# Kernel optimization log

Hardware: AMD Instinct MI355X
Metric: run time of the kernel (lower is better)

## Reference

```python
import jax, jax.numpy as jnp
import numpy as np

N_NODES = 50000
N_EDGES = 600000
N_REL = 64
D = 128
N_LAYERS = 2


def setup_inputs() -> dict:
    key = jax.random.key(0)
    k1, k2, k3, k4, k5, k6 = jax.random.split(key, 6)
    return {
        "entity_table": jax.random.normal(k1, (N_NODES, D), jnp.float32) * 0.05,
        "relation_table": jax.random.normal(k2, (N_REL, D), jnp.float32) * 0.05,
        "W": jax.random.normal(k3, (N_LAYERS, 2 * D, D), jnp.float32) * 0.05,
        "b": jnp.zeros((N_LAYERS, D), jnp.float32),
        "edge_dst": jax.random.randint(k4, (N_EDGES,), 0, N_NODES),
        "edge_nbr": jax.random.randint(k5, (N_EDGES,), 0, N_NODES),
        "edge_rel": jax.random.randint(k6, (N_EDGES,), 0, N_REL),
    }


def _segment_softmax(score, seg, num_segments):
    # numerically stable per-destination-node softmax over incoming edges
    smax = jax.ops.segment_max(score, seg, num_segments=num_segments)
    ex = jnp.exp(score - smax[seg])
    denom = jax.ops.segment_sum(ex, seg, num_segments=num_segments)
    return ex / denom[seg]


def reference(entity_table, relation_table, W, b, edge_dst, edge_nbr, edge_rel):
    n_nodes, d = entity_table.shape
    n_layers = W.shape[0]
    deg = jax.ops.segment_sum(jnp.ones_like(edge_dst, dtype=entity_table.dtype),
                              edge_dst, num_segments=n_nodes)
    has_nbr = (deg > 0)[:, None]  # [N,1]

    # relation-attentive query uses the BASE entity embedding of the dst node
    # (the torch code passes entity_embedder(current_node) each layer)
    q = jnp.tanh(entity_table[edge_dst] + relation_table[edge_rel])  # [E,d]

    prev = entity_table
    for l in range(n_layers):
        nbr_emb = prev[edge_nbr]                      # [E,d] gather
        score = jnp.sum(nbr_emb * q, axis=-1)         # [E]
        alpha = _segment_softmax(score, edge_dst, n_nodes)
        neigh = jax.ops.segment_sum(alpha[:, None] * nbr_emb, edge_dst,
                                    num_segments=n_nodes)  # [N,d]
        h = jnp.concatenate([prev, neigh], axis=-1) @ W[l] + b[l]
        h = jax.nn.leaky_relu(h)                      # LeakyReLU slope 0.01
        h = h / jnp.linalg.norm(h, axis=-1, keepdims=True)
        # nodes with no neighbours keep their base entity embedding
        prev = jnp.where(has_nbr, h, entity_table)
    return prev
```

## Files before the change

### kernel.cpp

```cpp
#include <hip/hip_runtime.h>
#include <math.h>

#define NN 50000
#define NE 600000
#define NR 64
#define DD 128
#define FB 586

typedef __attribute__((ext_vector_type(2))) _Float16 h2;
typedef __attribute__((ext_vector_type(4))) _Float16 h4;
typedef __attribute__((ext_vector_type(8))) _Float16 h8;
typedef __attribute__((ext_vector_type(4))) float f32x4;


__device__ __forceinline__ h2 tanh_h2(h2 x) {
    const h2 C5 = {(_Float16)0.1333333333f,  (_Float16)0.1333333333f};
    const h2 C3 = {(_Float16)-0.3333333333f, (_Float16)-0.3333333333f};
    const h2 ONE = {(_Float16)1.f, (_Float16)1.f};
    h2 x2 = x * x;
    h2 p = x2 * C5 + C3;
    p = x2 * p + ONE;
    return x * p;
}

template <int CTRL, int ROW_MASK>
__device__ __forceinline__ float dpp_add(float x) {
    int xi = __builtin_bit_cast(int, x);
    int yi = __builtin_amdgcn_update_dpp(0, xi, CTRL, ROW_MASK, 0xF, true);
    return x + __builtin_bit_cast(float, yi);
}


__global__ __launch_bounds__(256) void prep_k(const float* __restrict__ ent,
                                              const float* __restrict__ rel,
                                              const float* __restrict__ W,
                                              const int* __restrict__ edst,
                                              const int* __restrict__ enbr,
                                              const int* __restrict__ erel,
                                              _Float16* __restrict__ Ah,
                                              _Float16* __restrict__ relh,
                                              _Float16* __restrict__ wp,
                                              int* __restrict__ deg,
                                              int* __restrict__ bucket) {
    int b = blockIdx.x;
    if (b < FB) {
        int e = (b * 256 + threadIdx.x) * 4;
        if (e < NE) {
            int4 d  = *(const int4*)&edst[e];
            int4 nb = *(const int4*)&enbr[e];
            int4 rl = *(const int4*)&erel[e];
            int r0 = atomicAdd(&deg[d.x], 1);
            int r1 = atomicAdd(&deg[d.y], 1);
            int r2 = atomicAdd(&deg[d.z], 1);
            int r3 = atomicAdd(&deg[d.w], 1);
            if (r0 < 64) bucket[d.x * 64 + r0] = nb.x | (rl.x << 16);
            if (r1 < 64) bucket[d.y * 64 + r1] = nb.y | (rl.y << 16);
            if (r2 < 64) bucket[d.z * 64 + r2] = nb.z | (rl.z << 16);
            if (r3 < 64) bucket[d.w * 64 + r3] = nb.w | (rl.w << 16);
        }
    } else if (b < FB + 6250) {
        int tid = (b - FB) * 256 + threadIdx.x;
        int node = tid >> 5, c = tid & 31;
        float4 v = *(const float4*)&ent[(size_t)node * DD + c * 4];
        h4 o = {(_Float16)v.x, (_Float16)v.y, (_Float16)v.z, (_Float16)v.w};
        *(h4*)&Ah[(size_t)node * 256 + c * 4] = o;
    } else if (b < FB + 6258) {
        int tid = (b - FB - 6250) * 256 + threadIdx.x;
        float4 v = *(const float4*)&rel[tid * 4];
        h4 o = {(_Float16)v.x, (_Float16)v.y, (_Float16)v.z, (_Float16)v.w};
        *(h4*)&relh[tid * 4] = o;
    } else {
        int tid = (b - FB - 6258) * 256 + threadIdx.x;
        int lane = tid & 63;
        int ct   = (tid >> 6) & 7;
        int ks   = (tid >> 9) & 7;
        int l    = tid >> 12;
        int q = lane >> 4, n = lane & 15;
        const float* Wl = W + (size_t)l * 256 * 128;
        _Float16* dst = wp + ((((size_t)l * 8 + ks) * 8 + ct) * 64 + lane) * 8;
#pragma unroll
        for (int j = 0; j < 8; ++j) {
            int k = ks * 32 + q * 8 + j;
            dst[j] = (_Float16)Wl[(size_t)k * 128 + ct * 16 + n];
        }
    }
}


__global__ __launch_bounds__(256) void agg_k(const _Float16* __restrict__ Ah,
                                             const _Float16* __restrict__ Aq,
                                             const _Float16* __restrict__ relh,
                                             const int* __restrict__ deg_,
                                             const int* __restrict__ bucket,
                                             _Float16* __restrict__ Ah_out) {
    int lane = threadIdx.x & 63;
    int grp  = lane >> 4;
    int t16  = lane & 15;
    int wid  = threadIdx.x >> 6;
    int node = blockIdx.x * 4 + wid;
    int dg = deg_[node];

    unsigned dof = (unsigned)t16 * 8u;
    h8 qv = *(const h8*)&Aq[(unsigned)node * 256u + dof];
    h2 q0 = {qv[0], qv[1]}, q1 = {qv[2], qv[3]}, q2 = {qv[4], qv[5]}, q3 = {qv[6], qv[7]};

    float l = 0.f;
    h2 acc0 = {(_Float16)0.f, (_Float16)0.f};
    h2 acc1 = acc0, acc2 = acc0, acc3 = acc0;

    if (dg > 0) {
        int e0 = node * 64;
        int e1 = e0 + dg;
        int iters = (dg + 3) >> 2;
        int last = e1 - 1;
        int ei = e0 + grp;

        int pk_c = bucket[min(ei, last)];
        h8 nb_c = *(const h8*)&Ah[(unsigned)(pk_c & 0xFFFF) * 256u + dof];
        h8 rl_c = *(const h8*)&relh[(unsigned)(pk_c >> 16) * 128u + dof];
        int pk_n = bucket[min(ei + 4, last)];

#pragma unroll 2
        for (int it = 0; it < iters; ++it) {
            int pk_n2 = bucket[min(ei + 8, last)];
            h8 nb_n = *(const h8*)&Ah[(unsigned)(pk_n & 0xFFFF) * 256u + dof];
            h8 rl_n = *(const h8*)&relh[(unsigned)(pk_n >> 16) * 128u + dof];

            h2 n0 = {nb_c[0], nb_c[1]}, n1 = {nb_c[2], nb_c[3]};
            h2 n2 = {nb_c[4], nb_c[5]}, n3 = {nb_c[6], nb_c[7]};
            h2 r0 = {rl_c[0], rl_c[1]}, r1 = {rl_c[2], rl_c[3]};
            h2 r2 = {rl_c[4], rl_c[5]}, r3 = {rl_c[6], rl_c[7]};

            h2 sd = n0 * tanh_h2(q0 + r0);
            sd = n1 * tanh_h2(q1 + r1) + sd;
            sd = n2 * tanh_h2(q2 + r2) + sd;
            sd = n3 * tanh_h2(q3 + r3) + sd;
            float s = (float)sd.x + (float)sd.y;

            s = dpp_add<0x111, 0xF>(s);
            s = dpp_add<0x112, 0xF>(s);
            s = dpp_add<0x114, 0xF>(s);
            s = dpp_add<0x118, 0xF>(s);
            int si = __builtin_amdgcn_ds_swizzle(__builtin_bit_cast(int, s), 0x1F0);
            s = __builtin_bit_cast(float, si);

            float p = (ei < e1) ? __expf(s) : 0.f;
            l += p;
            _Float16 ph = (_Float16)p;
            h2 p2 = {ph, ph};
            acc0 = p2 * n0 + acc0;
            acc1 = p2 * n1 + acc1;
            acc2 = p2 * n2 + acc2;
            acc3 = p2 * n3 + acc3;

            ei += 4;
            pk_c = pk_n; pk_n = pk_n2;
            nb_c = nb_n; rl_c = rl_n;
        }

#pragma unroll
        for (int off = 16; off <= 32; off <<= 1) {
            acc0 += __builtin_bit_cast(h2, __shfl_xor(__builtin_bit_cast(int, acc0), off, 64));
            acc1 += __builtin_bit_cast(h2, __shfl_xor(__builtin_bit_cast(int, acc1), off, 64));
            acc2 += __builtin_bit_cast(h2, __shfl_xor(__builtin_bit_cast(int, acc2), off, 64));
            acc3 += __builtin_bit_cast(h2, __shfl_xor(__builtin_bit_cast(int, acc3), off, 64));
            l += __shfl_xor(l, off, 64);
        }
    }

    float inv = (dg > 0) ? __builtin_amdgcn_rcpf(l) : 0.f;
    if (grp == 0) {
        _Float16 ih = (_Float16)inv;
        h2 iv = {ih, ih};
        h2 o0 = acc0 * iv, o1 = acc1 * iv, o2 = acc2 * iv, o3 = acc3 * iv;
        h8 o = {o0.x, o0.y, o1.x, o1.y, o2.x, o2.y, o3.x, o3.y};
        *(h8*)&Ah_out[(unsigned)node * 256u + 128u + dof] = o;
    }
}


template <bool LAST>
__global__ __launch_bounds__(256) void upd_k(const _Float16* __restrict__ Ah,
                                             const _Float16* __restrict__ wp,
                                             const float* __restrict__ bl,
                                             const int* __restrict__ deg_,
                                             const float* __restrict__ ent,
                                             float* __restrict__ out,
                                             _Float16* __restrict__ Ahn) {
    int lane = threadIdx.x & 63, wid = threadIdx.x >> 6;
    int quad = lane >> 4, n16 = lane & 15;
    int row0 = (blockIdx.x * 4 + wid) * 16;
    int arow = min(row0 + n16, NN - 1);

    f32x4 acc[8];
#pragma unroll
    for (int ct = 0; ct < 8; ++ct) acc[ct] = (f32x4){0.f, 0.f, 0.f, 0.f};

    const h8* aptr = (const h8*)(Ah + (size_t)arow * 256 + quad * 8);
#pragma unroll
    for (int ks = 0; ks < 8; ++ks) {
        h8 af = aptr[ks * 4];
        const h8* bp = (const h8*)(wp + (((size_t)ks * 8) * 64 + lane) * 8);
#pragma unroll
        for (int ct = 0; ct < 8; ++ct) {
            h8 bfrag = bp[ct * 64];
            acc[ct] = __builtin_amdgcn_mfma_f32_16x16x32_f16(af, bfrag, acc[ct], 0, 0, 0);
        }
    }

    float bias[8];
#pragma unroll
    for (int ct = 0; ct < 8; ++ct) bias[ct] = bl[ct * 16 + n16];

#pragma unroll
    for (int r = 0; r < 4; ++r) {
        int orow = row0 + quad * 4 + r;
        float h[8];
        float ss = 0.f;
#pragma unroll
        for (int ct = 0; ct < 8; ++ct) {
            float v = acc[ct][r] + bias[ct];
            v = (v > 0.f) ? v : 0.01f * v;
            h[ct] = v;
            ss += v * v;
        }
        ss = dpp_add<0x111, 0xF>(ss);
        ss = dpp_add<0x112, 0xF>(ss);
        ss = dpp_add<0x114, 0xF>(ss);
        ss = dpp_add<0x118, 0xF>(ss);
        ss = __shfl(ss, 15, 16);
        float rinv = rsqrtf(ss);

        if (orow < NN) {
            bool iso = deg_[orow] == 0;
#pragma unroll
            for (int ct = 0; ct < 8; ++ct) {
                int col = ct * 16 + n16;
                float v = h[ct] * rinv;
                if (iso) v = ent[(size_t)orow * DD + col];
                if (LAST) out[(size_t)orow * DD + col] = v;
                else      Ahn[(size_t)orow * 256 + col] = (_Float16)v;
            }
        }
    }
}


extern "C" void kernel_launch(void* const* d_in, const int* in_sizes, int n_in,
                              void* d_out, int out_size, void* d_ws, size_t ws_size,
                              hipStream_t stream) {
    const float* ent = (const float*)d_in[0];
    const float* rel = (const float*)d_in[1];
    const float* W   = (const float*)d_in[2];
    const float* b   = (const float*)d_in[3];
    const int* edst  = (const int*)d_in[4];
    const int* enbr  = (const int*)d_in[5];
    const int* erel  = (const int*)d_in[6];
    float* out = (float*)d_out;

    char* ws = (char*)d_ws;
    size_t off = 0;
    auto alloc = [&](size_t bytes) -> void* {
        void* p = ws + off;
        off += (bytes + 255) & ~(size_t)255;
        return p;
    };
    int* deg       = (int*)alloc((size_t)NN * 4);
    int* bucket    = (int*)alloc((size_t)NN * 64 * 4);
    _Float16* Ah0  = (_Float16*)alloc((size_t)NN * 256 * 2);
    _Float16* Ah1  = (_Float16*)alloc((size_t)NN * 256 * 2);
    _Float16* wp   = (_Float16*)alloc((size_t)2 * 8 * 8 * 64 * 8 * 2);
    _Float16* relh = (_Float16*)alloc((size_t)NR * DD * 2);

    hipMemsetAsync(deg, 0, (size_t)NN * 4, stream);
    prep_k<<<FB + 6290, 256, 0, stream>>>(ent, rel, W, edst, enbr, erel,
                                          Ah0, relh, wp, deg, bucket);

    const _Float16* wp0 = wp;
    const _Float16* wp1 = wp + (size_t)8 * 8 * 64 * 8;
    int ublocks = (NN + 63) / 64;

    agg_k<<<NN / 4, 256, 0, stream>>>(Ah0, Ah0, relh, deg, bucket, Ah0);
    upd_k<false><<<ublocks, 256, 0, stream>>>(Ah0, wp0, b, deg, ent, out, Ah1);

    agg_k<<<NN / 4, 256, 0, stream>>>(Ah1, Ah0, relh, deg, bucket, Ah1);
    upd_k<true><<<ublocks, 256, 0, stream>>>(Ah1, wp1, b + DD, deg, ent, out, Ah0);
}
```

Before: 223.0 us.

## Partition edge bucketing into 8 per-block-class degree counters and compact layer buffers

Edge bucketing now uses 8 separate degree counter arrays selected by block index, each with 16 slots per node. This spreads atomic contention and shrinks the bucket footprint, and the aggregation kernel maps each edge index onto the right partition through prefix sums of the 8 partial degrees. The layer-1 node buffer shrinks to 128 halves per row, and the update kernel reads previous and aggregated features from separate buffers. The cost is extra index arithmetic per edge, 8 degree loads per node, and a 16-per-partition overflow cap that could drop edges when degrees are skewed.

Result: no change. 225.7 us (+1.2%).

```diff
diff --git a/kernel.cpp b/kernel.cpp
--- a/kernel.cpp
+++ b/kernel.cpp
@@ -6,6 +6,8 @@
 #define NR 64
 #define DD 128
 #define FB 586
+#define NP 8
+#define SL 16
 
 typedef __attribute__((ext_vector_type(2))) _Float16 h2;
 typedef __attribute__((ext_vector_type(4))) _Float16 h4;
@@ -40,23 +42,26 @@
                                               _Float16* __restrict__ Ah,
                                               _Float16* __restrict__ relh,
                                               _Float16* __restrict__ wp,
-                                              int* __restrict__ deg,
+                                              int* __restrict__ deg8,
                                               int* __restrict__ bucket) {
     int b = blockIdx.x;
     if (b < FB) {
+        int p = b & (NP - 1);
         int e = (b * 256 + threadIdx.x) * 4;
         if (e < NE) {
             int4 d  = *(const int4*)&edst[e];
             int4 nb = *(const int4*)&enbr[e];
             int4 rl = *(const int4*)&erel[e];
-            int r0 = atomicAdd(&deg[d.x], 1);
-            int r1 = atomicAdd(&deg[d.y], 1);
-            int r2 = atomicAdd(&deg[d.z], 1);
-            int r3 = atomicAdd(&deg[d.w], 1);
-            if (r0 < 64) bucket[d.x * 64 + r0] = nb.x | (rl.x << 16);
-            if (r1 < 64) bucket[d.y * 64 + r1] = nb.y | (rl.y << 16);
-            if (r2 < 64) bucket[d.z * 64 + r2] = nb.z | (rl.z << 16);
-            if (r3 < 64) bucket[d.w * 64 + r3] = nb.w | (rl.w << 16);
+            int* degp = deg8 + (size_t)p * NN;
+            int bp = p * NN;
+            int r0 = atomicAdd(&degp[d.x], 1);
+            int r1 = atomicAdd(&degp[d.y], 1);
+            int r2 = atomicAdd(&degp[d.z], 1);
+            int r3 = atomicAdd(&degp[d.w], 1);
+            if (r0 < SL) bucket[((bp + d.x) << 4) + r0] = nb.x | (rl.x << 16);
+            if (r1 < SL) bucket[((bp + d.y) << 4) + r1] = nb.y | (rl.y << 16);
+            if (r2 < SL) bucket[((bp + d.z) << 4) + r2] = nb.z | (rl.z << 16);
+            if (r3 < SL) bucket[((bp + d.w) << 4) + r3] = nb.w | (rl.w << 16);
         }
     } else if (b < FB + 6250) {
         int tid = (b - FB) * 256 + threadIdx.x;
@@ -87,18 +92,41 @@
 }
 
 
-__global__ __launch_bounds__(256) void agg_k(const _Float16* __restrict__ Ah,
+__device__ __forceinline__ int remap_j(int j, int node,
+                                       int d0, int d1, int d2, int d3,
+                                       int d4, int d5, int d6) {
+    int s = d0, xb = 0, base = 0;
+    if (j >= s) { xb += NN * SL; base = s; }
+    s += d1; if (j >= s) { xb += NN * SL; base = s; }
+    s += d2; if (j >= s) { xb += NN * SL; base = s; }
+    s += d3; if (j >= s) { xb += NN * SL; base = s; }
+    s += d4; if (j >= s) { xb += NN * SL; base = s; }
+    s += d5; if (j >= s) { xb += NN * SL; base = s; }
+    s += d6; if (j >= s) { xb += NN * SL; base = s; }
+    int off = j - base;
+    off = (off < SL) ? off : (SL - 1);
+    return xb + node * SL + off;
+}
+
+template <int NBS>
+__global__ __launch_bounds__(256) void agg_k(const _Float16* __restrict__ nbuf,
                                              const _Float16* __restrict__ Aq,
                                              const _Float16* __restrict__ relh,
-                                             const int* __restrict__ deg_,
+                                             const int* __restrict__ deg8,
                                              const int* __restrict__ bucket,
-                                             _Float16* __restrict__ Ah_out) {
+                                             int* __restrict__ deg_tot,
+                                             _Float16* __restrict__ aggout) {
     int lane = threadIdx.x & 63;
     int grp  = lane >> 4;
     int t16  = lane & 15;
     int wid  = threadIdx.x >> 6;
     int node = blockIdx.x * 4 + wid;
-    int dg = deg_[node];
+
+    const int* dgp = deg8 + node;
+    int d0 = dgp[0], d1 = dgp[NN], d2 = dgp[2 * NN], d3 = dgp[3 * NN];
+    int d4 = dgp[4 * NN], d5 = dgp[5 * NN], d6 = dgp[6 * NN], d7 = dgp[7 * NN];
+    int dg = d0 + d1 + d2 + d3 + d4 + d5 + d6 + d7;
+    if (lane == 0) deg_tot[node] = dg;
 
     unsigned dof = (unsigned)t16 * 8u;
     h8 qv = *(const h8*)&Aq[(unsigned)node * 256u + dof];
@@ -109,22 +137,22 @@
     h2 acc1 = acc0, acc2 = acc0, acc3 = acc0;
 
     if (dg > 0) {
-        int e0 = node * 64;
-        int e1 = e0 + dg;
         int iters = (dg + 3) >> 2;
-        int last = e1 - 1;
-        int ei = e0 + grp;
-
-        int pk_c = bucket[min(ei, last)];
-        h8 nb_c = *(const h8*)&Ah[(unsigned)(pk_c & 0xFFFF) * 256u + dof];
-        h8 rl_c = *(const h8*)&relh[(unsigned)(pk_c >> 16) * 128u + dof];
-        int pk_n = bucket[min(ei + 4, last)];
+        int last = dg - 1;
+        int j = grp;
+
+        int pk_c = bucket[remap_j(min(j, last), node, d0, d1, d2, d3, d4, d5, d6)];
+        unsigned ni_c = min((unsigned)(pk_c & 0xFFFF), (unsigned)(NN - 1));
+        h8 nb_c = *(const h8*)&nbuf[ni_c * (unsigned)NBS + dof];
+        h8 rl_c = *(const h8*)&relh[(unsigned)((pk_c >> 16) & 63) * 128u + dof];
+        int pk_n = bucket[remap_j(min(j + 4, last), node, d0, d1, d2, d3, d4, d5, d6)];
 
 #pragma unroll 2
         for (int it = 0; it < iters; ++it) {
-            int pk_n2 = bucket[min(ei + 8, last)];
-            h8 nb_n = *(const h8*)&Ah[(unsigned)(pk_n & 0xFFFF) * 256u + dof];
-            h8 rl_n = *(const h8*)&relh[(unsigned)(pk_n >> 16) * 128u + dof];
+            int pk_n2 = bucket[remap_j(min(j + 8, last), node, d0, d1, d2, d3, d4, d5, d6)];
+            unsigned ni_n = min((unsigned)(pk_n & 0xFFFF), (unsigned)(NN - 1));
+            h8 nb_n = *(const h8*)&nbuf[ni_n * (unsigned)NBS + dof];
+            h8 rl_n = *(const h8*)&relh[(unsigned)((pk_n >> 16) & 63) * 128u + dof];
 
             h2 n0 = {nb_c[0], nb_c[1]}, n1 = {nb_c[2], nb_c[3]};
             h2 n2 = {nb_c[4], nb_c[5]}, n3 = {nb_c[6], nb_c[7]};
@@ -144,7 +172,7 @@
             int si = __builtin_amdgcn_ds_swizzle(__builtin_bit_cast(int, s), 0x1F0);
             s = __builtin_bit_cast(float, si);
 
-            float p = (ei < e1) ? __expf(s) : 0.f;
+            float p = (j < dg) ? __expf(s) : 0.f;
             l += p;
             _Float16 ph = (_Float16)p;
             h2 p2 = {ph, ph};
@@ -153,7 +181,7 @@
             acc2 = p2 * n2 + acc2;
             acc3 = p2 * n3 + acc3;
 
-            ei += 4;
+            j += 4;
             pk_c = pk_n; pk_n = pk_n2;
             nb_c = nb_n; rl_c = rl_n;
         }
@@ -174,16 +202,17 @@
         h2 iv = {ih, ih};
         h2 o0 = acc0 * iv, o1 = acc1 * iv, o2 = acc2 * iv, o3 = acc3 * iv;
         h8 o = {o0.x, o0.y, o1.x, o1.y, o2.x, o2.y, o3.x, o3.y};
-        *(h8*)&Ah_out[(unsigned)node * 256u + 128u + dof] = o;
-    }
-}
-
-
-template <bool LAST>
-__global__ __launch_bounds__(256) void upd_k(const _Float16* __restrict__ Ah,
+        *(h8*)&aggout[(unsigned)node * 256u + 128u + dof] = o;
+    }
+}
+
+
+template <bool LAST, int SP>
+__global__ __launch_bounds__(256) void upd_k(const _Float16* __restrict__ prev,
+                                             const _Float16* __restrict__ agg,
                                              const _Float16* __restrict__ wp,
                                              const float* __restrict__ bl,
-                                             const int* __restrict__ deg_,
+                                             const int* __restrict__ deg_tot,
                                              const float* __restrict__ ent,
                                              float* __restrict__ out,
                                              _Float16* __restrict__ Ahn) {
@@ -196,10 +225,11 @@
 #pragma unroll
     for (int ct = 0; ct < 8; ++ct) acc[ct] = (f32x4){0.f, 0.f, 0.f, 0.f};
 
-    const h8* aptr = (const h8*)(Ah + (size_t)arow * 256 + quad * 8);
+    const h8* apP = (const h8*)(prev + (size_t)arow * SP + quad * 8);
+    const h8* apQ = (const h8*)(agg + (size_t)arow * 256 + 128 + quad * 8);
 #pragma unroll
     for (int ks = 0; ks < 8; ++ks) {
-        h8 af = aptr[ks * 4];
+        h8 af = (ks < 4) ? apP[ks * 4] : apQ[(ks - 4) * 4];
         const h8* bp = (const h8*)(wp + (((size_t)ks * 8) * 64 + lane) * 8);
 #pragma unroll
         for (int ct = 0; ct < 8; ++ct) {
@@ -232,14 +262,14 @@
         float rinv = rsqrtf(ss);
 
         if (orow < NN) {
-            bool iso = deg_[orow] == 0;
+            bool iso = deg_tot[orow] == 0;
 #pragma unroll
             for (int ct = 0; ct < 8; ++ct) {
                 int col = ct * 16 + n16;
                 float v = h[ct] * rinv;
                 if (iso) v = ent[(size_t)orow * DD + col];
                 if (LAST) out[(size_t)orow * DD + col] = v;
-                else      Ahn[(size_t)orow * 256 + col] = (_Float16)v;
+                else      Ahn[(size_t)orow * 128 + col] = (_Float16)v;
             }
         }
     }
@@ -265,24 +295,25 @@
         off += (bytes + 255) & ~(size_t)255;
         return p;
     };
-    int* deg       = (int*)alloc((size_t)NN * 4);
-    int* bucket    = (int*)alloc((size_t)NN * 64 * 4);
+    int* deg8      = (int*)alloc((size_t)NN * NP * 4);
+    int* deg_tot   = (int*)alloc((size_t)NN * 4);
+    int* bucket    = (int*)alloc((size_t)NN * NP * SL * 4);
     _Float16* Ah0  = (_Float16*)alloc((size_t)NN * 256 * 2);
-    _Float16* Ah1  = (_Float16*)alloc((size_t)NN * 256 * 2);
+    _Float16* Ah1  = (_Float16*)alloc((size_t)NN * 128 * 2);
     _Float16* wp   = (_Float16*)alloc((size_t)2 * 8 * 8 * 64 * 8 * 2);
     _Float16* relh = (_Float16*)alloc((size_t)NR * DD * 2);
 
-    hipMemsetAsync(deg, 0, (size_t)NN * 4, stream);
+    hipMemsetAsync(deg8, 0, (size_t)NN * NP * 4, stream);
     prep_k<<<FB + 6290, 256, 0, stream>>>(ent, rel, W, edst, enbr, erel,
-                                          Ah0, relh, wp, deg, bucket);
+                                          Ah0, relh, wp, deg8, bucket);
 
     const _Float16* wp0 = wp;
     const _Float16* wp1 = wp + (size_t)8 * 8 * 64 * 8;
     int ublocks = (NN + 63) / 64;
 
-    agg_k<<<NN / 4, 256, 0, stream>>>(Ah0, Ah0, relh, deg, bucket, Ah0);
-    upd_k<false><<<ublocks, 256, 0, stream>>>(Ah0, wp0, b, deg, ent, out, Ah1);
-
-    agg_k<<<NN / 4, 256, 0, stream>>>(Ah1, Ah0, relh, deg, bucket, Ah1);
-    upd_k<true><<<ublocks, 256, 0, stream>>>(Ah1, wp1, b + DD, deg, ent, out, Ah0);
-}
+    agg_k<256><<<NN / 4, 256, 0, stream>>>(Ah0, Ah0, relh, deg8, bucket, deg_tot, Ah0);
+    upd_k<false, 256><<<ublocks, 256, 0, stream>>>(Ah0, Ah0, wp0, b, deg_tot, ent, out, Ah1);
+
+    agg_k<128><<<NN / 4, 256, 0, stream>>>(Ah1, Ah0, relh, deg8, bucket, deg_tot, Ah0);
+    upd_k<true, 128><<<ublocks, 256, 0, stream>>>(Ah1, Ah0, wp1, b + DD, deg_tot, ent, out, Ah1);
+}
```
